# Performance work log

Hardware: AMD Instinct MI355X
Metric: run time of the kernel (lower is better)

## Reference

```python
import jax, jax.numpy as jnp
import numpy as np

FG_THRESH = 0.5
BG_THRESH = 0.4
REG_W = (10.0, 10.0, 5.0, 5.0)
SMOOTH_L1_BETA = 1.0 / 9.0


def box_iou(a, b):
    # a: [G,4], b: [T,4] -> [G,T]
    area_a = (a[:, 2] - a[:, 0]) * (a[:, 3] - a[:, 1])
    area_b = (b[:, 2] - b[:, 0]) * (b[:, 3] - b[:, 1])
    lt = jnp.maximum(a[:, None, :2], b[None, :, :2])
    rb = jnp.minimum(a[:, None, 2:], b[None, :, 2:])
    wh = jnp.clip(rb - lt, 0.0)
    inter = wh[..., 0] * wh[..., 1]
    return inter / (area_a[:, None] + area_b[None, :] - inter)


def elementwise_iou(a, b):
    # a, b: [T,4] -> [T]
    area_a = (a[:, 2] - a[:, 0]) * (a[:, 3] - a[:, 1])
    area_b = (b[:, 2] - b[:, 0]) * (b[:, 3] - b[:, 1])
    lt = jnp.maximum(a[:, :2], b[:, :2])
    rb = jnp.minimum(a[:, 2:], b[:, 2:])
    wh = jnp.clip(rb - lt, 0.0)
    inter = wh[:, 0] * wh[:, 1]
    return inter / (area_a + area_b - inter)


def encode_boxes(ref_boxes, proposals):
    # torchvision BoxCoder.encode with weights (10,10,5,5)
    wx, wy, ww, wh = REG_W
    ex_w = proposals[:, 2] - proposals[:, 0]
    ex_h = proposals[:, 3] - proposals[:, 1]
    ex_cx = proposals[:, 0] + 0.5 * ex_w
    ex_cy = proposals[:, 1] + 0.5 * ex_h
    gt_w = ref_boxes[:, 2] - ref_boxes[:, 0]
    gt_h = ref_boxes[:, 3] - ref_boxes[:, 1]
    gt_cx = ref_boxes[:, 0] + 0.5 * gt_w
    gt_cy = ref_boxes[:, 1] + 0.5 * gt_h
    dx = wx * (gt_cx - ex_cx) / ex_w
    dy = wy * (gt_cy - ex_cy) / ex_h
    dw = ww * jnp.log(gt_w / ex_w)
    dh = wh * jnp.log(gt_h / ex_h)
    return jnp.stack([dx, dy, dw, dh], axis=1)


def _match_and_targets(all_props, gtb, gtl):
    # all_props: [T,4], gtb: [G,4], gtl: [G]
    iou = box_iou(gtb, all_props)                       # [G,T]
    matched_vals = jnp.max(iou, axis=0)                 # [T]
    matched_idxs = jnp.argmax(iou, axis=0)              # [T] (clamped match)
    labels = gtl[matched_idxs].astype(jnp.int32)
    labels = jnp.where(matched_vals < BG_THRESH, 0, labels)          # background
    labels = jnp.where((matched_vals >= BG_THRESH) & (matched_vals < FG_THRESH), -1, labels)  # ignore
    matched_gt = gtb[matched_idxs]                      # [T,4]
    reg_targets = encode_boxes(matched_gt, all_props)   # [T,4]
    score_targets = elementwise_iou(matched_gt, all_props)  # [T]
    return labels, reg_targets, score_targets


def _losses(proposals, gt_boxes, gt_labels, class_logits, box_regression, box_scores):
    B = proposals.shape[0]
    # add_gt_proposals: concat gt boxes onto proposals
    all_props = jnp.concatenate([proposals, gt_boxes], axis=1)  # [B,T,4]
    labels, reg_t, bs_t = jax.vmap(_match_and_targets)(all_props, gt_boxes, gt_labels)

    C = class_logits.shape[-1]
    N = B * class_logits.shape[1]
    labels = labels.reshape(-1)                         # [N]
    logits = class_logits.reshape(N, C)
    breg = box_regression.reshape(N, C, 4)
    bsc = box_scores.reshape(-1)
    reg_t = reg_t.reshape(N, 4)
    bs_t = bs_t.reshape(-1)

    valid = labels >= 0
    pos = labels > 0
    n_valid = jnp.maximum(jnp.sum(valid), 1).astype(logits.dtype)
    n_pos = jnp.maximum(jnp.sum(pos), 1).astype(logits.dtype)
    safe_lab = jnp.clip(labels, 0, C - 1)

    # classification: cross-entropy over non-ignored rois
    logp = jax.nn.log_softmax(logits, axis=-1)
    nll = -jnp.take_along_axis(logp, safe_lab[:, None], axis=1)[:, 0]
    cls_loss = jnp.sum(jnp.where(valid, nll, 0.0)) / n_valid

    pred_reg = jnp.take_along_axis(breg, safe_lab[:, None, None], axis=1)[:, 0]  # [N,4]
    diff = jnp.abs(pred_reg - reg_t)
    sl1 = jnp.where(diff < SMOOTH_L1_BETA, 0.5 * diff * diff / SMOOTH_L1_BETA, diff - 0.5 * SMOOTH_L1_BETA)
    box_loss = jnp.sum(jnp.where(pos[:, None], sl1, 0.0)) / n_valid

    # box score: L1 between predicted score and IoU target on positives
    score_loss = jnp.sum(jnp.where(pos, jnp.abs(bsc - bs_t), 0.0)) / n_pos

    return jnp.stack([cls_loss, box_loss, score_loss])


def setup_inputs() -> dict:
    key = jax.random.key(0)
    ks = jax.random.split(key, 6)
    B, P, G, C = 8, 8000, 100, 81

    def make_boxes(k, shape):
        k1, k2, k3, k4 = jax.random.split(k, 4)
        x1 = jax.random.uniform(k1, shape) * 800.0
        y1 = jax.random.uniform(k2, shape) * 600.0
        w = 8.0 + jax.random.uniform(k3, shape) * 192.0
        h = 8.0 + jax.random.uniform(k4, shape) * 192.0
        return jnp.stack([x1, y1, x1 + w, y1 + h], axis=-1)

    return {
        "proposals": make_boxes(ks[0], (B, P)),
        "gt_boxes": make_boxes(ks[1], (B, G)),
        "gt_labels": jax.random.randint(ks[2], (B, G), 1, C),
        "class_logits": jax.random.normal(ks[3], (B, P + G, C), dtype=jnp.float32),
        "box_regression": jax.random.normal(ks[4], (B, P + G, C * 4), dtype=jnp.float32) * 0.1,
        "box_scores": jax.random.uniform(ks[5], (B, P + G)),
    }


def reference(proposals, gt_boxes, gt_labels, class_logits, box_regression, box_scores):
    return _losses(proposals, gt_boxes, gt_labels, class_logits, box_regression, box_scores)
```

## Files before the change

### kernel.cpp

```cpp
#include <hip/hip_runtime.h>
#include <math.h>

namespace {
constexpr int kB = 8;
constexpr int kP = 8000;
constexpr int kG = 100;
constexpr int kT = kP + kG;
constexpr int kC = 81;
constexpr int kBlk = 512;
constexpr int kLanes = 16;
constexpr int kGroups = kBlk / kLanes;
constexpr int kRowsPerBlock = 2 * kGroups;
constexpr int kBlocksPerBatch = (kT + kRowsPerBlock - 1) / kRowsPerBlock;
constexpr int kNBlk = kB * kBlocksPerBatch;
constexpr int kStride = 1024;
constexpr float kFG = 0.5f;
constexpr float kBG = 0.4f;
constexpr float kBeta = 1.0f / 9.0f;
}

template <int C>
__device__ __forceinline__ float dppf(float v) {
  return __int_as_float(
      __builtin_amdgcn_update_dpp(0, __float_as_int(v), C, 0xF, 0xF, true));
}
template <int C>
__device__ __forceinline__ int dppi(int v) {
  return __builtin_amdgcn_update_dpp(0, v, C, 0xF, 0xF, true);
}
#define ROR8 0x128
#define ROR4 0x124
#define ROR2 0x122
#define ROR1 0x121

__global__ __launch_bounds__(kBlk, 8) void roi_partials(
    const float* __restrict__ proposals,
    const float* __restrict__ gt_boxes,
    const int*   __restrict__ gt_labels,
    const float* __restrict__ class_logits,
    const float* __restrict__ box_reg,
    const float* __restrict__ box_scores,
    float* __restrict__ partials)
{
  __shared__ float4 s_gt[kG];
  __shared__ float  s_area[kG];
  __shared__ int    s_lab[kG];
  __shared__ float  s_red[kBlk / 64][5];

  const int l   = threadIdx.x & (kLanes - 1);
  const int grp = threadIdx.x >> 4;
  const int b   = blockIdx.y;

  for (int i = threadIdx.x; i < kG; i += kBlk) {
    const float4 g = reinterpret_cast<const float4*>(gt_boxes)[(size_t)b * kG + i];
    s_gt[i] = g;
    s_area[i] = (g.z - g.x) * (g.w - g.y);
    s_lab[i] = gt_labels[b * kG + i];
  }
  __syncthreads();

  float a_nll = 0.f, a_sl1 = 0.f, a_sc = 0.f, a_cv = 0.f, a_cp = 0.f;

  #pragma unroll
  for (int tile = 0; tile < 2; ++tile) {
    const int t = blockIdx.x * kRowsPerBlock + tile * kGroups + grp;
    if (t < kT) {
      const size_t r = (size_t)b * kT + t;
      const float4 pb = (t < kP)
          ? reinterpret_cast<const float4*>(proposals)[(size_t)b * kP + t]
          : s_gt[t - kP];
      float x[6];
      const float* lg = class_logits + r * kC;
      #pragma unroll
      for (int k = 0; k < 5; ++k) x[k] = lg[l + k * kLanes];
      x[5] = (l == 0) ? lg[80] : -INFINITY;
      const float bs = (l == 0) ? box_scores[r] : 0.f;

      const float area_p = (pb.z - pb.x) * (pb.w - pb.y);

      float best = -1.f;
      int bi = 0;
      #pragma unroll
      for (int k = 0; k < 7; ++k) {
        const int g = l + k * kLanes;
        if (k < 6 || g < kG) {
          const float4 gb = s_gt[g];
          float w = fminf(gb.z, pb.z) - fmaxf(gb.x, pb.x);
          float h = fminf(gb.w, pb.w) - fmaxf(gb.y, pb.y);
          w = fmaxf(w, 0.f);
          h = fmaxf(h, 0.f);
          const float inter = w * h;
          const float iou =
              inter * __builtin_amdgcn_rcpf(s_area[g] + area_p - inter);
          if (iou > best) { best = iou; bi = g; }
        }
      }
      #define ARGMAX_STEP(C)                                                 \
        {                                                                    \
          const float ob = dppf<C>(best);                                    \
          const int   oi = dppi<C>(bi);                                      \
          if (ob > best || (ob == best && oi < bi)) { best = ob; bi = oi; }  \
        }
      ARGMAX_STEP(ROR8)
      ARGMAX_STEP(ROR4)
      ARGMAX_STEP(ROR2)
      ARGMAX_STEP(ROR1)
      #undef ARGMAX_STEP

      int label = s_lab[bi];
      if (best < kBG) label = 0;
      else if (best < kFG) label = -1;
      const bool valid = label >= 0;
      const bool pos = label > 0;
      const int lab = valid ? label : 0;

      float se = 0.f;
      #pragma unroll
      for (int k = 0; k < 6; ++k) se += __expf(x[k]);
      se += dppf<ROR8>(se);
      se += dppf<ROR4>(se);
      se += dppf<ROR2>(se);
      se += dppf<ROR1>(se);
      if (valid && l == 0) {
        const float xl = lg[lab];
        a_nll += __logf(se) - xl;
        a_cv += 1.f;
      }

      if (pos && l == 0) {
        const float4 gb = s_gt[bi];
        const float ex_w = pb.z - pb.x, ex_h = pb.w - pb.y;
        const float ex_cx = pb.x + 0.5f * ex_w, ex_cy = pb.y + 0.5f * ex_h;
        const float gt_w = gb.z - gb.x, gt_h = gb.w - gb.y;
        const float gt_cx = gb.x + 0.5f * gt_w, gt_cy = gb.y + 0.5f * gt_h;
        const float tx = 10.f * (gt_cx - ex_cx) / ex_w;
        const float ty = 10.f * (gt_cy - ex_cy) / ex_h;
        const float tw = 5.f * __logf(gt_w / ex_w);
        const float th = 5.f * __logf(gt_h / ex_h);
        const float4 pv =
            reinterpret_cast<const float4*>(box_reg)[r * kC + lab];
        const float d0 = fabsf(pv.x - tx), d1 = fabsf(pv.y - ty);
        const float d2 = fabsf(pv.z - tw), d3 = fabsf(pv.w - th);
        float s = 0.f;
        s += (d0 < kBeta) ? 4.5f * d0 * d0 : d0 - 0.5f * kBeta;
        s += (d1 < kBeta) ? 4.5f * d1 * d1 : d1 - 0.5f * kBeta;
        s += (d2 < kBeta) ? 4.5f * d2 * d2 : d2 - 0.5f * kBeta;
        s += (d3 < kBeta) ? 4.5f * d3 * d3 : d3 - 0.5f * kBeta;
        a_sl1 += s;
        a_sc += fabsf(bs - best);
        a_cp += 1.f;
      }
    }
  }

  float vals[5] = {a_nll, a_sl1, a_sc, a_cv, a_cp};
  #pragma unroll
  for (int j = 0; j < 5; ++j) {
    vals[j] += __shfl_down(vals[j], 32, 64);
    vals[j] += __shfl_down(vals[j], 16, 64);
  }
  const int wave = threadIdx.x >> 6, lane = threadIdx.x & 63;
  if (lane == 0) {
    #pragma unroll
    for (int j = 0; j < 5; ++j) s_red[wave][j] = vals[j];
  }
  __syncthreads();
  if (threadIdx.x == 0) {
    const int slot = blockIdx.y * kBlocksPerBatch + blockIdx.x;
    #pragma unroll
    for (int j = 0; j < 5; ++j) {
      float tot = 0.f;
      #pragma unroll
      for (int w = 0; w < kBlk / 64; ++w) tot += s_red[w][j];
      partials[j * kStride + slot] = tot;
    }
  }
}

__global__ __launch_bounds__(1024) void roi_finalize(
    const float* __restrict__ partials, float* __restrict__ out) {
  __shared__ float s_red[16][5];
  float vals[5] = {0.f, 0.f, 0.f, 0.f, 0.f};
  if (threadIdx.x < kNBlk) {
    #pragma unroll
    for (int j = 0; j < 5; ++j) vals[j] = partials[j * kStride + threadIdx.x];
  }
  #pragma unroll
  for (int off = 32; off > 0; off >>= 1) {
    #pragma unroll
    for (int j = 0; j < 5; ++j) vals[j] += __shfl_down(vals[j], off, 64);
  }
  const int wave = threadIdx.x >> 6, lane = threadIdx.x & 63;
  if (lane == 0) {
    #pragma unroll
    for (int j = 0; j < 5; ++j) s_red[wave][j] = vals[j];
  }
  __syncthreads();
  if (threadIdx.x == 0) {
    float tot[5];
    #pragma unroll
    for (int j = 0; j < 5; ++j) {
      float s = 0.f;
      #pragma unroll
      for (int w = 0; w < 16; ++w) s += s_red[w][j];
      tot[j] = s;
    }
    const float nv = fmaxf(tot[3], 1.f);
    const float np = fmaxf(tot[4], 1.f);
    out[0] = tot[0] / nv;
    out[1] = tot[1] / nv;
    out[2] = tot[2] / np;
  }
}

extern "C" void kernel_launch(void* const* d_in, const int* in_sizes, int n_in,
                              void* d_out, int out_size, void* d_ws, size_t ws_size,
                              hipStream_t stream) {
  (void)in_sizes; (void)n_in; (void)out_size; (void)ws_size;
  const float* proposals    = (const float*)d_in[0];
  const float* gt_boxes     = (const float*)d_in[1];
  const int*   gt_labels    = (const int*)d_in[2];
  const float* class_logits = (const float*)d_in[3];
  const float* box_reg      = (const float*)d_in[4];
  const float* box_scores   = (const float*)d_in[5];
  float* partials = (float*)d_ws;
  float* out = (float*)d_out;

  dim3 grid(kBlocksPerBatch, kB);
  roi_partials<<<grid, kBlk, 0, stream>>>(proposals, gt_boxes, gt_labels,
                                          class_logits, box_reg, box_scores,
                                          partials);
  roi_finalize<<<1, 1024, 0, stream>>>(partials, out);
}
```

Baseline: 18.30 us.

## Interleave IoU argmax for both rows, pad GT table, and double block size

Each thread now computes the IoU argmax for both of its rows in one interleaved loop, with the proposal loads issued before the shared-memory GT setup. The GT table is padded to 112 zero boxes so the inner loop carries no bounds branch. Blocks grow from 512 to 1024 threads, so there are half as many partial sums and the finalize kernel shrinks to 512 threads with unconditional loads. The aim is more instruction-level parallelism and less control flow. In exchange, register pressure rises, and the logits loads now come after the IoU work, which may leave their latency less hidden.

```diff
diff --git a/kernel.cpp b/kernel.cpp
--- a/kernel.cpp
+++ b/kernel.cpp
@@ -5,15 +5,16 @@
 constexpr int kB = 8;
 constexpr int kP = 8000;
 constexpr int kG = 100;
+constexpr int kGPad = 112;
 constexpr int kT = kP + kG;
 constexpr int kC = 81;
-constexpr int kBlk = 512;
+constexpr int kBlk = 1024;
 constexpr int kLanes = 16;
 constexpr int kGroups = kBlk / kLanes;
 constexpr int kRowsPerBlock = 2 * kGroups;
 constexpr int kBlocksPerBatch = (kT + kRowsPerBlock - 1) / kRowsPerBlock;
 constexpr int kNBlk = kB * kBlocksPerBatch;
-constexpr int kStride = 1024;
+constexpr int kStride = 512;
 constexpr float kFG = 0.5f;
 constexpr float kBG = 0.4f;
 constexpr float kBeta = 1.0f / 9.0f;
@@ -42,114 +43,143 @@
     const float* __restrict__ box_scores,
     float* __restrict__ partials)
 {
-  __shared__ float4 s_gt[kG];
-  __shared__ float  s_area[kG];
+  __shared__ float4 s_gt[kGPad];
+  __shared__ float  s_area[kGPad];
   __shared__ int    s_lab[kG];
   __shared__ float  s_red[kBlk / 64][5];
 
   const int l   = threadIdx.x & (kLanes - 1);
   const int grp = threadIdx.x >> 4;
   const int b   = blockIdx.y;
-
-  for (int i = threadIdx.x; i < kG; i += kBlk) {
-    const float4 g = reinterpret_cast<const float4*>(gt_boxes)[(size_t)b * kG + i];
+  const int t0  = blockIdx.x * kRowsPerBlock + grp;
+  const int t1  = t0 + kGroups;
+  const bool in0 = t0 < kT;
+  const bool in1 = t1 < kT;
+  const size_t r0 = (size_t)b * kT + t0;
+  const size_t r1 = (size_t)b * kT + t1;
+
+  float4 pb0 = make_float4(0.f, 0.f, 1.f, 1.f);
+  float4 pb1 = make_float4(0.f, 0.f, 1.f, 1.f);
+  if (in0 && t0 < kP)
+    pb0 = reinterpret_cast<const float4*>(proposals)[(size_t)b * kP + t0];
+  if (in1 && t1 < kP)
+    pb1 = reinterpret_cast<const float4*>(proposals)[(size_t)b * kP + t1];
+
+  for (int i = threadIdx.x; i < kGPad; i += kBlk) {
+    float4 g = make_float4(0.f, 0.f, 0.f, 0.f);
+    if (i < kG)
+      g = reinterpret_cast<const float4*>(gt_boxes)[(size_t)b * kG + i];
     s_gt[i] = g;
     s_area[i] = (g.z - g.x) * (g.w - g.y);
-    s_lab[i] = gt_labels[b * kG + i];
+    if (i < kG) s_lab[i] = gt_labels[b * kG + i];
   }
   __syncthreads();
+  if (in0 && t0 >= kP) pb0 = s_gt[t0 - kP];
+  if (in1 && t1 >= kP) pb1 = s_gt[t1 - kP];
+
+  const float ap0 = (pb0.z - pb0.x) * (pb0.w - pb0.y);
+  const float ap1 = (pb1.z - pb1.x) * (pb1.w - pb1.y);
+
+  float best0 = -1.f, best1 = -1.f;
+  int bi0 = 0, bi1 = 0;
+  #pragma unroll
+  for (int k = 0; k < 7; ++k) {
+    const int g = l + k * kLanes;
+    const float4 gb = s_gt[g];
+    const float ga = s_area[g];
+    {
+      float w = fminf(gb.z, pb0.z) - fmaxf(gb.x, pb0.x);
+      float h = fminf(gb.w, pb0.w) - fmaxf(gb.y, pb0.y);
+      w = fmaxf(w, 0.f);
+      h = fmaxf(h, 0.f);
+      const float inter = w * h;
+      const float iou = inter * __builtin_amdgcn_rcpf(ga + ap0 - inter);
+      if (iou > best0) { best0 = iou; bi0 = g; }
+    }
+    {
+      float w = fminf(gb.z, pb1.z) - fmaxf(gb.x, pb1.x);
+      float h = fminf(gb.w, pb1.w) - fmaxf(gb.y, pb1.y);
+      w = fmaxf(w, 0.f);
+      h = fmaxf(h, 0.f);
+      const float inter = w * h;
+      const float iou = inter * __builtin_amdgcn_rcpf(ga + ap1 - inter);
+      if (iou > best1) { best1 = iou; bi1 = g; }
+    }
+  }
+  #define ARGMAX_STEP(C, best, bi)                                        \
+    {                                                                     \
+      const float ob = dppf<C>(best);                                     \
+      const int   oi = dppi<C>(bi);                                       \
+      if (ob > best || (ob == best && oi < bi)) { best = ob; bi = oi; }   \
+    }
+  ARGMAX_STEP(ROR8, best0, bi0)
+  ARGMAX_STEP(ROR4, best0, bi0)
+  ARGMAX_STEP(ROR2, best0, bi0)
+  ARGMAX_STEP(ROR1, best0, bi0)
+  ARGMAX_STEP(ROR8, best1, bi1)
+  ARGMAX_STEP(ROR4, best1, bi1)
+  ARGMAX_STEP(ROR2, best1, bi1)
+  ARGMAX_STEP(ROR1, best1, bi1)
+  #undef ARGMAX_STEP
 
   float a_nll = 0.f, a_sl1 = 0.f, a_sc = 0.f, a_cv = 0.f, a_cp = 0.f;
 
   #pragma unroll
   for (int tile = 0; tile < 2; ++tile) {
-    const int t = blockIdx.x * kRowsPerBlock + tile * kGroups + grp;
-    if (t < kT) {
-      const size_t r = (size_t)b * kT + t;
-      const float4 pb = (t < kP)
-          ? reinterpret_cast<const float4*>(proposals)[(size_t)b * kP + t]
-          : s_gt[t - kP];
-      float x[6];
-      const float* lg = class_logits + r * kC;
-      #pragma unroll
-      for (int k = 0; k < 5; ++k) x[k] = lg[l + k * kLanes];
-      x[5] = (l == 0) ? lg[80] : -INFINITY;
-      const float bs = (l == 0) ? box_scores[r] : 0.f;
-
-      const float area_p = (pb.z - pb.x) * (pb.w - pb.y);
-
-      float best = -1.f;
-      int bi = 0;
-      #pragma unroll
-      for (int k = 0; k < 7; ++k) {
-        const int g = l + k * kLanes;
-        if (k < 6 || g < kG) {
-          const float4 gb = s_gt[g];
-          float w = fminf(gb.z, pb.z) - fmaxf(gb.x, pb.x);
-          float h = fminf(gb.w, pb.w) - fmaxf(gb.y, pb.y);
-          w = fmaxf(w, 0.f);
-          h = fmaxf(h, 0.f);
-          const float inter = w * h;
-          const float iou =
-              inter * __builtin_amdgcn_rcpf(s_area[g] + area_p - inter);
-          if (iou > best) { best = iou; bi = g; }
-        }
-      }
-      #define ARGMAX_STEP(C)                                                 \
-        {                                                                    \
-          const float ob = dppf<C>(best);                                    \
-          const int   oi = dppi<C>(bi);                                      \
-          if (ob > best || (ob == best && oi < bi)) { best = ob; bi = oi; }  \
-        }
-      ARGMAX_STEP(ROR8)
-      ARGMAX_STEP(ROR4)
-      ARGMAX_STEP(ROR2)
-      ARGMAX_STEP(ROR1)
-      #undef ARGMAX_STEP
-
-      int label = s_lab[bi];
-      if (best < kBG) label = 0;
-      else if (best < kFG) label = -1;
-      const bool valid = label >= 0;
-      const bool pos = label > 0;
-      const int lab = valid ? label : 0;
-
-      float se = 0.f;
-      #pragma unroll
-      for (int k = 0; k < 6; ++k) se += __expf(x[k]);
-      se += dppf<ROR8>(se);
-      se += dppf<ROR4>(se);
-      se += dppf<ROR2>(se);
-      se += dppf<ROR1>(se);
-      if (valid && l == 0) {
-        const float xl = lg[lab];
-        a_nll += __logf(se) - xl;
-        a_cv += 1.f;
-      }
-
-      if (pos && l == 0) {
-        const float4 gb = s_gt[bi];
-        const float ex_w = pb.z - pb.x, ex_h = pb.w - pb.y;
-        const float ex_cx = pb.x + 0.5f * ex_w, ex_cy = pb.y + 0.5f * ex_h;
-        const float gt_w = gb.z - gb.x, gt_h = gb.w - gb.y;
-        const float gt_cx = gb.x + 0.5f * gt_w, gt_cy = gb.y + 0.5f * gt_h;
-        const float tx = 10.f * (gt_cx - ex_cx) / ex_w;
-        const float ty = 10.f * (gt_cy - ex_cy) / ex_h;
-        const float tw = 5.f * __logf(gt_w / ex_w);
-        const float th = 5.f * __logf(gt_h / ex_h);
-        const float4 pv =
-            reinterpret_cast<const float4*>(box_reg)[r * kC + lab];
-        const float d0 = fabsf(pv.x - tx), d1 = fabsf(pv.y - ty);
-        const float d2 = fabsf(pv.z - tw), d3 = fabsf(pv.w - th);
-        float s = 0.f;
-        s += (d0 < kBeta) ? 4.5f * d0 * d0 : d0 - 0.5f * kBeta;
-        s += (d1 < kBeta) ? 4.5f * d1 * d1 : d1 - 0.5f * kBeta;
-        s += (d2 < kBeta) ? 4.5f * d2 * d2 : d2 - 0.5f * kBeta;
-        s += (d3 < kBeta) ? 4.5f * d3 * d3 : d3 - 0.5f * kBeta;
-        a_sl1 += s;
-        a_sc += fabsf(bs - best);
-        a_cp += 1.f;
-      }
+    const bool in = tile ? in1 : in0;
+    if (!in) continue;
+    const size_t r = tile ? r1 : r0;
+    const float best = tile ? best1 : best0;
+    const int bi = tile ? bi1 : bi0;
+    const float4 pb = tile ? pb1 : pb0;
+
+    int label = s_lab[bi];
+    if (best < kBG) label = 0;
+    else if (best < kFG) label = -1;
+    const bool valid = label >= 0;
+    const bool pos = label > 0;
+    const int lab = valid ? label : 0;
+
+    const float* lg = class_logits + r * kC;
+    float x[6];
+    #pragma unroll
+    for (int k = 0; k < 5; ++k) x[k] = lg[l + k * kLanes];
+    x[5] = (l == 0) ? lg[80] : -INFINITY;
+    float se = 0.f;
+    #pragma unroll
+    for (int k = 0; k < 6; ++k) se += __expf(x[k]);
+    se += dppf<ROR8>(se);
+    se += dppf<ROR4>(se);
+    se += dppf<ROR2>(se);
+    se += dppf<ROR1>(se);
+    if (valid && l == 0) {
+      const float xl = lg[lab];
+      a_nll += __logf(se) - xl;
+      a_cv += 1.f;
+    }
+
+    if (pos && l == 0) {
+      const float4 gb = s_gt[bi];
+      const float ex_w = pb.z - pb.x, ex_h = pb.w - pb.y;
+      const float ex_cx = pb.x + 0.5f * ex_w, ex_cy = pb.y + 0.5f * ex_h;
+      const float gt_w = gb.z - gb.x, gt_h = gb.w - gb.y;
+      const float gt_cx = gb.x + 0.5f * gt_w, gt_cy = gb.y + 0.5f * gt_h;
+      const float tx = 10.f * (gt_cx - ex_cx) / ex_w;
+      const float ty = 10.f * (gt_cy - ex_cy) / ex_h;
+      const float tw = 5.f * __logf(gt_w / ex_w);
+      const float th = 5.f * __logf(gt_h / ex_h);
+      const float4 pv =
+          reinterpret_cast<const float4*>(box_reg)[r * kC + lab];
+      const float d0 = fabsf(pv.x - tx), d1 = fabsf(pv.y - ty);
+      const float d2 = fabsf(pv.z - tw), d3 = fabsf(pv.w - th);
+      float s = 0.f;
+      s += (d0 < kBeta) ? 4.5f * d0 * d0 : d0 - 0.5f * kBeta;
+      s += (d1 < kBeta) ? 4.5f * d1 * d1 : d1 - 0.5f * kBeta;
+      s += (d2 < kBeta) ? 4.5f * d2 * d2 : d2 - 0.5f * kBeta;
+      s += (d3 < kBeta) ? 4.5f * d3 * d3 : d3 - 0.5f * kBeta;
+      a_sl1 += s;
+      a_sc += fabsf(box_scores[r] - best);
+      a_cp += 1.f;
     }
   }
 
@@ -177,14 +207,12 @@
   }
 }
 
-__global__ __launch_bounds__(1024) void roi_finalize(
+__global__ __launch_bounds__(512) void roi_finalize(
     const float* __restrict__ partials, float* __restrict__ out) {
-  __shared__ float s_red[16][5];
-  float vals[5] = {0.f, 0.f, 0.f, 0.f, 0.f};
-  if (threadIdx.x < kNBlk) {
-    #pragma unroll
-    for (int j = 0; j < 5; ++j) vals[j] = partials[j * kStride + threadIdx.x];
-  }
+  __shared__ float s_red[8][5];
+  float vals[5];
+  #pragma unroll
+  for (int j = 0; j < 5; ++j) vals[j] = partials[j * kStride + threadIdx.x];
   #pragma unroll
   for (int off = 32; off > 0; off >>= 1) {
     #pragma unroll
@@ -202,7 +230,7 @@
     for (int j = 0; j < 5; ++j) {
       float s = 0.f;
       #pragma unroll
-      for (int w = 0; w < 16; ++w) s += s_red[w][j];
+      for (int w = 0; w < 8; ++w) s += s_red[w][j];
       tot[j] = s;
     }
     const float nv = fmaxf(tot[3], 1.f);
@@ -230,5 +258,5 @@
   roi_partials<<<grid, kBlk, 0, stream>>>(proposals, gt_boxes, gt_labels,
                                           class_logits, box_reg, box_scores,
                                           partials);
-  roi_finalize<<<1, 1024, 0, stream>>>(partials, out);
-}
+  roi_finalize<<<1, 512, 0, stream>>>(partials, out);
+}
```

New measurement: 17.58 us. 3.9% less time.
